# Optimization experiments

Hardware: AMD Instinct MI355X
Metric: run time of the kernel (lower is better)

## Reference

```python
import jax, jax.numpy as jnp
import numpy as np

N, M1, M2 = 8, 512, 512
NITER = 6
LAM = 0.1
BETA = 4096
WL = 6.37e-07  # wavelength constant from expjQz


def _c(x):
    # [..., 2] float (real, imag) -> complex
    return jax.lax.complex(x[..., 0], x[..., 1])


def _ri(x):
    # complex -> [..., 2] float
    return jnp.stack([jnp.real(x), jnp.imag(x)], axis=-1)


def _fft2(x):
    return jnp.fft.fft2(x, axes=(-2, -1))


def _ifft2(x):
    return jnp.fft.ifft2(x, axes=(-2, -1))


def _conv(x, T):
    # Convolve.apply: frequency-domain multiplication by transfer function T (M1,M2)
    return _ifft2(_fft2(x) * T)


def _normalize(x):
    # project onto unit magnitude (phase-only), guarding zero magnitude
    m = jnp.abs(x)
    return x / jnp.where(m == 0, 1.0, m)


def _forward(inp, Q, z):
    # T = exp(1j * z/WL * Q), the expjQz transfer function
    T = jnp.exp(1j * (z / WL) * Q)  # complex64, (M1, M2)
    H = _c(inp)                      # (N, M1, M2) complex measurements
    B = _fft2(jnp.ones((N, M1, M2), jnp.complex64))   # B0 = fft2(ones)
    X = jnp.zeros((N, M1, M2), jnp.complex64)          # X0 = 0
    W = jnp.ones((N, M1, M2), jnp.complex64)           # W0 = 1
    for i in range(NITER):
        convXT = _conv(X, T)
        W = _normalize(convXT + _ifft2(B))
        Qc = H * W
        B = _fft2(Qc - convXT)
        # top-beta magnitude support selection on flattened |B|
        vals, _ = jax.lax.top_k(jnp.abs(B).reshape(-1), BETA)
        thr = vals[-1]
        B = B * (jnp.abs(B) >= thr)
        inp1 = _conv(Qc - _ifft2(B), jnp.conj(T))
        if i < NITER - 1:
            X = inp1 * (jnp.abs(inp1) > LAM)
        else:
            X = inp1
    return W, B


def setup_inputs() -> dict:
    key = jax.random.key(0)
    k1, k2 = jax.random.split(key)
    inp = jax.random.normal(k1, (N, M1, M2, 2), dtype=jnp.float32)
    Q = jax.random.normal(k2, (M1, M2), dtype=jnp.float32)
    z = jnp.float32(1e-06)
    return {"input": inp, "Q": Q, "z": z}


def reference(input, Q, z):
    W, B = _forward(input, Q, z)
    # return real/imag-stacked outputs (aux_W, squeeze(aux_B))
    return _ri(W).astype(jnp.float32), _ri(B).astype(jnp.float32)
```

## Files before the change

### kernel.cpp

```cpp
#include <hip/hip_runtime.h>
#include <math.h>

#define NIMG 8
#define MDIM 512
#define IMGE (MDIM*MDIM)
#define TOT  (NIMG*IMGE)
#define BETA_K 4096
#define LAMD 0.1

typedef double2 c64;

struct SelState { unsigned int known; unsigned int rank; unsigned int thrkey; };

__device__ __forceinline__ int LPOS(int ln, int q){
    return (ln << 9) + (q ^ ((((q >> 4) ^ (2 * ln)) & 7) << 1));
}
__device__ __forceinline__ int rev8(int n){
    return ((n & 7) << 6) | (n & 56) | (n >> 6);
}
__device__ __forceinline__ int rde(int w, int k){
    return 64*k + 8*(w & 7) + (w >> 3);
}

template<bool INV>
__device__ __forceinline__ void dft8(double* xr, double* xi){
    const double C = 0.70710678118654752440;
    double t0r=xr[0]+xr[4], t0i=xi[0]+xi[4];
    double t1r=xr[0]-xr[4], t1i=xi[0]-xi[4];
    double t2r=xr[2]+xr[6], t2i=xi[2]+xi[6];
    double t3r=xr[2]-xr[6], t3i=xi[2]-xi[6];
    double m3r = INV ? -t3i : t3i;
    double m3i = INV ?  t3r : -t3r;
    double E0r=t0r+t2r, E0i=t0i+t2i;
    double E2r=t0r-t2r, E2i=t0i-t2i;
    double E1r=t1r+m3r, E1i=t1i+m3i;
    double E3r=t1r-m3r, E3i=t1i-m3i;
    double u0r=xr[1]+xr[5], u0i=xi[1]+xi[5];
    double u1r=xr[1]-xr[5], u1i=xi[1]-xi[5];
    double u2r=xr[3]+xr[7], u2i=xi[3]+xi[7];
    double u3r=xr[3]-xr[7], u3i=xi[3]-xi[7];
    double n3r = INV ? -u3i : u3i;
    double n3i = INV ?  u3r : -u3r;
    double O0r=u0r+u2r, O0i=u0i+u2i;
    double O2r=u0r-u2r, O2i=u0i-u2i;
    double O1r=u1r+n3r, O1i=u1i+n3i;
    double O3r=u1r-n3r, O3i=u1i-n3i;
    double W1r = INV ? C*(O1r - O1i) : C*(O1r + O1i);
    double W1i = INV ? C*(O1r + O1i) : C*(O1i - O1r);
    double W2r = INV ? -O2i : O2i;
    double W2i = INV ?  O2r : -O2r;
    double W3r = INV ? -C*(O3r + O3i) : C*(O3i - O3r);
    double W3i = INV ?  C*(O3r - O3i) : -C*(O3r + O3i);
    xr[0]=E0r+O0r; xi[0]=E0i+O0i;  xr[4]=E0r-O0r; xi[4]=E0i-O0i;
    xr[1]=E1r+W1r; xi[1]=E1i+W1i;  xr[5]=E1r-W1r; xi[5]=E1i-W1i;
    xr[2]=E2r+W2r; xi[2]=E2i+W2i;  xr[6]=E2r-W2r; xi[6]=E2i-W2i;
    xr[3]=E3r+W3r; xi[3]=E3i+W3i;  xr[7]=E3r-W3r; xi[7]=E3i-W3i;
}

template<bool INV>
__device__ __forceinline__ void dit_from_regs(double (&ar)[2][8], double (&ai)[2][8],
                                              double* re, double* im, const c64* __restrict__ tw){
    const int t=threadIdx.x, w=t&63, l0=t>>6;
    #pragma unroll
    for (int h=0;h<2;++h){
        dft8<INV>(ar[h], ai[h]);
        const int ln=l0+4*h;
        #pragma unroll
        for (int k=0;k<8;++k){ int p=LPOS(ln,8*w+k); re[p]=ar[h][k]; im[p]=ai[h][k]; }
    }
    __syncthreads();
    {
        const int g=w>>3, j=w&7;
        double wr[8], wi[8];
        #pragma unroll
        for (int k=1;k<8;++k){ c64 tv=tw[8*j*k]; wr[k]=tv.x; wi[k]=INV?-tv.y:tv.y; }
        #pragma unroll
        for (int h=0;h<2;++h){
            const int ln=l0+4*h;
            double xr[8], xi[8];
            #pragma unroll
            for (int k=0;k<8;++k){ int p=LPOS(ln,64*g+j+8*k); double a=re[p],b=im[p];
                if(k==0){xr[0]=a; xi[0]=b;} else {xr[k]=a*wr[k]-b*wi[k]; xi[k]=a*wi[k]+b*wr[k];} }
            dft8<INV>(xr,xi);
            #pragma unroll
            for (int k=0;k<8;++k){ int p=LPOS(ln,64*g+j+8*k); re[p]=xr[k]; im[p]=xi[k]; }
        }
    }
    __syncthreads();
    {
        const int j=w;
        double wr[8], wi[8];
        #pragma unroll
        for (int k=1;k<8;++k){ c64 tv=tw[j*k]; wr[k]=tv.x; wi[k]=INV?-tv.y:tv.y; }
        #pragma unroll
        for (int h=0;h<2;++h){
            const int ln=l0+4*h;
            #pragma unroll
            for (int k=0;k<8;++k){ int p=LPOS(ln,j+64*k); double a=re[p],b=im[p];
                if(k==0){ar[h][0]=a; ai[h][0]=b;} else {ar[h][k]=a*wr[k]-b*wi[k]; ai[h][k]=a*wi[k]+b*wr[k];} }
            dft8<INV>(ar[h], ai[h]);
        }
    }
}

template<bool INV>
__device__ __forceinline__ void dif_to_regs(double (&ar)[2][8], double (&ai)[2][8],
                                            double* re, double* im, const c64* __restrict__ tw){
    const int t=threadIdx.x, w=t&63, l0=t>>6;
    {
        const int j=w;
        double wr[8], wi[8];
        #pragma unroll
        for (int k=1;k<8;++k){ c64 tv=tw[j*k]; wr[k]=tv.x; wi[k]=INV?-tv.y:tv.y; }
        #pragma unroll
        for (int h=0;h<2;++h){
            dft8<INV>(ar[h], ai[h]);
            const int ln=l0+4*h;
            #pragma unroll
            for (int k=0;k<8;++k){
                int p=LPOS(ln,j+64*k);
                if(k==0){ re[p]=ar[h][0]; im[p]=ai[h][0]; }
                else { re[p]=ar[h][k]*wr[k]-ai[h][k]*wi[k]; im[p]=ar[h][k]*wi[k]+ai[h][k]*wr[k]; }
            }
        }
    }
    __syncthreads();
    {
        const int g=w>>3, j=w&7;
        double wr[8], wi[8];
        #pragma unroll
        for (int k=1;k<8;++k){ c64 tv=tw[8*j*k]; wr[k]=tv.x; wi[k]=INV?-tv.y:tv.y; }
        #pragma unroll
        for (int h=0;h<2;++h){
            const int ln=l0+4*h;
            double xr[8], xi[8];
            #pragma unroll
            for (int k=0;k<8;++k){ int p=LPOS(ln,64*g+j+8*k); xr[k]=re[p]; xi[k]=im[p]; }
            dft8<INV>(xr,xi);
            #pragma unroll
            for (int k=0;k<8;++k){
                int p=LPOS(ln,64*g+j+8*k);
                if(k==0){ re[p]=xr[0]; im[p]=xi[0]; }
                else { re[p]=xr[k]*wr[k]-xi[k]*wi[k]; im[p]=xr[k]*wi[k]+xi[k]*wr[k]; }
            }
        }
    }
    __syncthreads();
    #pragma unroll
    for (int h=0;h<2;++h){
        const int ln=l0+4*h;
        #pragma unroll
        for (int k=0;k<8;++k){ int p=LPOS(ln,8*w+k); ar[h][k]=re[p]; ai[h][k]=im[p]; }
        dft8<INV>(ar[h], ai[h]);
    }
}

template<bool INV>
__device__ void r8_dit(double* re, double* im, const c64* __restrict__ tw){
    const int t = threadIdx.x;
    const int w = t & 63;
    const int l0 = t >> 6;
    __syncthreads();
    #pragma unroll
    for (int h = 0; h < 2; ++h){
        const int ln = l0 + 4*h;
        double xr[8], xi[8];
        #pragma unroll
        for (int k = 0; k < 8; ++k){ int p = LPOS(ln, 8*w + k); xr[k]=re[p]; xi[k]=im[p]; }
        dft8<INV>(xr, xi);
        #pragma unroll
        for (int k = 0; k < 8; ++k){ int p = LPOS(ln, 8*w + k); re[p]=xr[k]; im[p]=xi[k]; }
    }
    {
        const int g = w >> 3, j = w & 7;
        double wr[8], wi[8];
        #pragma unroll
        for (int k = 1; k < 8; ++k){ c64 tv = tw[8*j*k]; wr[k]=tv.x; wi[k]= INV ? -tv.y : tv.y; }
        __syncthreads();
        #pragma unroll
        for (int h = 0; h < 2; ++h){
            const int ln = l0 + 4*h;
            double xr[8], xi[8];
            #pragma unroll
            for (int k = 0; k < 8; ++k){
                int p = LPOS(ln, 64*g + j + 8*k); double ar=re[p], ai=im[p];
                if (k == 0){ xr[0]=ar; xi[0]=ai; }
                else { xr[k]=ar*wr[k]-ai*wi[k]; xi[k]=ar*wi[k]+ai*wr[k]; }
            }
            dft8<INV>(xr, xi);
            #pragma unroll
            for (int k = 0; k < 8; ++k){ int p = LPOS(ln, 64*g + j + 8*k); re[p]=xr[k]; im[p]=xi[k]; }
        }
    }
    {
        const int j = w;
        double wr[8], wi[8];
        #pragma unroll
        for (int k = 1; k < 8; ++k){ c64 tv = tw[j*k]; wr[k]=tv.x; wi[k]= INV ? -tv.y : tv.y; }
        __syncthreads();
        #pragma unroll
        for (int h = 0; h < 2; ++h){
            const int ln = l0 + 4*h;
            double xr[8], xi[8];
            #pragma unroll
            for (int k = 0; k < 8; ++k){
                int p = LPOS(ln, j + 64*k); double ar=re[p], ai=im[p];
                if (k == 0){ xr[0]=ar; xi[0]=ai; }
                else { xr[k]=ar*wr[k]-ai*wi[k]; xi[k]=ar*wi[k]+ai*wr[k]; }
            }
            dft8<INV>(xr, xi);
            #pragma unroll
            for (int k = 0; k < 8; ++k){ int p = LPOS(ln, j + 64*k); re[p]=xr[k]; im[p]=xi[k]; }
        }
    }
}

template<bool INV>
__device__ void r8_dif(double* re, double* im, const c64* __restrict__ tw){
    const int t = threadIdx.x;
    const int w = t & 63;
    const int l0 = t >> 6;
    {
        const int j = w;
        double wr[8], wi[8];
        #pragma unroll
        for (int k = 1; k < 8; ++k){ c64 tv = tw[j*k]; wr[k]=tv.x; wi[k]= INV ? -tv.y : tv.y; }
        __syncthreads();
        #pragma unroll
        for (int h = 0; h < 2; ++h){
            const int ln = l0 + 4*h;
            double xr[8], xi[8];
            #pragma unroll
            for (int k = 0; k < 8; ++k){ int p = LPOS(ln, j + 64*k); xr[k]=re[p]; xi[k]=im[p]; }
            dft8<INV>(xr, xi);
            #pragma unroll
            for (int k = 0; k < 8; ++k){
                int p = LPOS(ln, j + 64*k);
                if (k == 0){ re[p]=xr[0]; im[p]=xi[0]; }
                else { re[p]=xr[k]*wr[k]-xi[k]*wi[k]; im[p]=xr[k]*wi[k]+xi[k]*wr[k]; }
            }
        }
    }
    {
        const int g = w >> 3, j = w & 7;
        double wr[8], wi[8];
        #pragma unroll
        for (int k = 1; k < 8; ++k){ c64 tv = tw[8*j*k]; wr[k]=tv.x; wi[k]= INV ? -tv.y : tv.y; }
        __syncthreads();
        #pragma unroll
        for (int h = 0; h < 2; ++h){
            const int ln = l0 + 4*h;
            double xr[8], xi[8];
            #pragma unroll
            for (int k = 0; k < 8; ++k){ int p = LPOS(ln, 64*g + j + 8*k); xr[k]=re[p]; xi[k]=im[p]; }
            dft8<INV>(xr, xi);
            #pragma unroll
            for (int k = 0; k < 8; ++k){
                int p = LPOS(ln, 64*g + j + 8*k);
                if (k == 0){ re[p]=xr[0]; im[p]=xi[0]; }
                else { re[p]=xr[k]*wr[k]-xi[k]*wi[k]; im[p]=xr[k]*wi[k]+xi[k]*wr[k]; }
            }
        }
    }
    __syncthreads();
    #pragma unroll
    for (int h = 0; h < 2; ++h){
        const int ln = l0 + 4*h;
        double xr[8], xi[8];
        #pragma unroll
        for (int k = 0; k < 8; ++k){ int p = LPOS(ln, 8*w + k); xr[k]=re[p]; xi[k]=im[p]; }
        dft8<INV>(xr, xi);
        #pragma unroll
        for (int k = 0; k < 8; ++k){ int p = LPOS(ln, 8*w + k); re[p]=xr[k]; im[p]=xi[k]; }
    }
}

__device__ __forceinline__ void col_load32(const float2* __restrict__ src, size_t base,
                                           double* re, double* im){
    const int t = threadIdx.x;
    #pragma unroll
    for (int it = 0; it < 16; ++it){
        int idx = it*256 + t; int ln = idx & 7, e = idx >> 3;
        float2 v = src[base + ln + (size_t)e*512];
        int p = LPOS(ln, rev8(e));
        re[p] = (double)v.x; im[p] = (double)v.y;
    }
}

__global__ __launch_bounds__(256) void k_init(const float* __restrict__ Q,
                                              const float* __restrict__ zp,
                                              c64* __restrict__ T,
                                              c64* __restrict__ tw){
    int i = blockIdx.x*256 + threadIdx.x;
    if (i < IMGE){
        double a = ((double)zp[0] / 6.37e-07) * (double)Q[i];
        T[i] = make_double2(cos(a), sin(a));
    }
    if (i < 512){
        double a = -6.283185307179586476925286766559 * ((double)i / 512.0);
        tw[i] = make_double2(cos(a), sin(a));
    }
}

__global__ __launch_bounds__(256,2) void k_colF(const float2* __restrict__ H,
                                                float2* __restrict__ t2,
                                                const c64* __restrict__ tw){
    __shared__ double re[4096]; __shared__ double im[4096];
    const int t = threadIdx.x, blk = blockIdx.x;
    const size_t base = (size_t)(blk >> 6) * IMGE + (size_t)(blk & 63) * 8;
    col_load32(H, base, re, im);
    r8_dit<false>(re, im, tw);
    __syncthreads();
    #pragma unroll
    for (int it = 0; it < 16; ++it){
        int idx = it*256 + t; int ln = idx & 7, e = idx >> 3;
        int p = LPOS(ln, e);
        t2[base + ln + (size_t)e*512] = make_float2((float)re[p], (float)im[p]);
    }
}

__global__ __launch_bounds__(256,2) void k_rowA(const float2* __restrict__ B,
                                                const unsigned int* __restrict__ keys,
                                                const SelState* __restrict__ st,
                                                const float2* __restrict__ G,
                                                float2* __restrict__ t2,
                                                const c64* __restrict__ tw){
    __shared__ double re[4096]; __shared__ double im[4096];
    const int t = threadIdx.x, blk = blockIdx.x;
    const int w = t & 63, l0 = t >> 6;
    const size_t base = (size_t)blk * 4096;
    const unsigned int thr = st->thrkey;
    double ar[2][8], ai[2][8];
    #pragma unroll
    for (int h=0;h<2;++h){ const int ln=l0+4*h;
        #pragma unroll
        for (int k=0;k<8;++k){
            size_t addr = base + ln*512 + (w + 64*k);
            float2 g = G[addr];
            float2 b = B[addr];
            bool keep = keys[addr] >= thr;
            ar[h][k] = (double)g.x + (keep ? (double)b.x : 0.0);
            ai[h][k] = (double)g.y + (keep ? (double)b.y : 0.0);
        } }
    dif_to_regs<true>(ar, ai, re, im, tw);
    const double sc = 1.0/512.0;
    #pragma unroll
    for (int h=0;h<2;++h){ const int ln=l0+4*h;
        #pragma unroll
        for (int k=0;k<8;++k)
            t2[base + ln*512 + rde(w,k)] = make_float2((float)(ar[h][k]*sc), (float)(ai[h][k]*sc)); }
}

template<bool FINAL>
__global__ __launch_bounds__(256,2) void k_colWQ(float2* __restrict__ t2,
                                                 const float2* __restrict__ H,
                                                 float2* __restrict__ outW,
                                                 const c64* __restrict__ tw){
    __shared__ double re[4096]; __shared__ double im[4096];
    const int t = threadIdx.x, blk = blockIdx.x;
    const size_t base = (size_t)(blk >> 6) * IMGE + (size_t)(blk & 63) * 8;
    col_load32(t2, base, re, im);
    r8_dit<true>(re, im, tw);
    __syncthreads();
    const double sc = 1.0/512.0;
    #pragma unroll
    for (int it = 0; it < 16; ++it){
        int idx = it*256 + t; int ln = idx & 7, e = idx >> 3;
        size_t addr = base + ln + (size_t)e*512;
        int p = LPOS(ln, e);
        double zr = re[p]*sc, zi = im[p]*sc;
        double m = sqrt(zr*zr + zi*zi);
        double d = (m == 0.0) ? 1.0 : m;
        double wx = zr/d, wy = zi/d;
        if (FINAL) outW[addr] = make_float2((float)wx, (float)wy);
        float2 h = H[addr];
        re[p] = (double)h.x*wx - (double)h.y*wy;
        im[p] = (double)h.x*wy + (double)h.y*wx;
    }
    r8_dif<false>(re, im, tw);
    __syncthreads();
    #pragma unroll
    for (int it = 0; it < 16; ++it){
        int idx = it*256 + t; int ln = idx & 7, e = idx >> 3;
        int p = LPOS(ln, rev8(e));
        t2[base + ln + (size_t)e*512] = make_float2((float)re[p], (float)im[p]);
    }
}

template<bool G0>
__global__ __launch_bounds__(256,2) void k_rowC(const float2* __restrict__ t2,
                                                const float2* __restrict__ G,
                                                float2* __restrict__ B,
                                                unsigned int* __restrict__ keys,
                                                unsigned int* __restrict__ hist,
                                                const c64* __restrict__ tw){
    __shared__ double re[4096]; __shared__ double im[4096];
    const int t = threadIdx.x, blk = blockIdx.x;
    const int w = t & 63, l0 = t >> 6;
    const size_t base = (size_t)blk * 4096;
    double ar[2][8], ai[2][8];
    #pragma unroll
    for (int h=0;h<2;++h){ const int ln=l0+4*h;
        #pragma unroll
        for (int k=0;k<8;++k){ float2 v = t2[base + ln*512 + rde(w,k)];
            ar[h][k]=(double)v.x; ai[h][k]=(double)v.y; } }
    dit_from_regs<false>(ar, ai, re, im, tw);
    __syncthreads();
    unsigned int* lh = reinterpret_cast<unsigned int*>(re);
    for (int b = t; b < 2048; b += 256) lh[b] = 0u;
    __syncthreads();
    #pragma unroll
    for (int h=0;h<2;++h){
        const int ln=l0+4*h;
        #pragma unroll
        for (int k=0;k<8;++k){
            size_t addr = base + ln*512 + (w + 64*k);
            double br = ar[h][k], bi = ai[h][k];
            if (!G0){ float2 g = G[addr]; br -= (double)g.x; bi -= (double)g.y; }
            B[addr] = make_float2((float)br, (float)bi);
            unsigned int key = __float_as_uint((float)sqrt(br*br + bi*bi));
            keys[addr] = key;
            atomicAdd(&lh[key >> 21], 1u);
        }
    }
    __syncthreads();
    for (int b = t; b < 2048; b += 256){
        unsigned int v = lh[b];
        if (v) atomicAdd(&hist[b], v);
    }
}

template<bool G0>
__global__ __launch_bounds__(256,2) void k_rowD(const float2* __restrict__ B,
                                                const unsigned int* __restrict__ keys,
                                                const SelState* __restrict__ st,
                                                const float2* __restrict__ G,
                                                const c64* __restrict__ T,
                                                float2* __restrict__ t2,
                                                const c64* __restrict__ tw){
    __shared__ double re[4096]; __shared__ double im[4096];
    const int t = threadIdx.x, blk = blockIdx.x;
    const int w = t & 63, l0 = t >> 6;
    const size_t base = (size_t)blk * 4096;
    const unsigned int thr = st->thrkey;
    double ar[2][8], ai[2][8];
    #pragma unroll
    for (int h=0;h<2;++h){
        const int ln=l0+4*h;
        const int u = (blk & 63) * 8 + ln;
        #pragma unroll
        for (int k=0;k<8;++k){
            const int e = w + 64*k;
            size_t addr = base + ln*512 + e;
            float2 b = B[addr];
            bool lo = keys[addr] < thr;
            double vr = lo ? (double)b.x : 0.0;
            double vi = lo ? (double)b.y : 0.0;
            if (!G0){ float2 g = G[addr]; vr += (double)g.x; vi += (double)g.y; }
            c64 tv = T[u*512 + e];
            ar[h][k] = vr*tv.x + vi*tv.y;
            ai[h][k] = vi*tv.x - vr*tv.y;
        }
    }
    dif_to_regs<true>(ar, ai, re, im, tw);
    const double sc = 1.0/512.0;
    #pragma unroll
    for (int h=0;h<2;++h){ const int ln=l0+4*h;
        #pragma unroll
        for (int k=0;k<8;++k)
            t2[base + ln*512 + rde(w,k)] = make_float2((float)(ar[h][k]*sc), (float)(ai[h][k]*sc)); }
}

__global__ __launch_bounds__(256,2) void k_colX(float2* __restrict__ t2,
                                                const c64* __restrict__ tw){
    __shared__ double re[4096]; __shared__ double im[4096];
    const int t = threadIdx.x, blk = blockIdx.x;
    const size_t base = (size_t)(blk >> 6) * IMGE + (size_t)(blk & 63) * 8;
    col_load32(t2, base, re, im);
    r8_dit<true>(re, im, tw);
    __syncthreads();
    const double sc = 1.0/512.0;
    #pragma unroll
    for (int it = 0; it < 16; ++it){
        int idx = it*256 + t;
        int p = LPOS(idx & 7, idx >> 3);
        double vr = re[p]*sc, vi = im[p]*sc;
        double m = sqrt(vr*vr + vi*vi);
        bool keep = m > LAMD;
        re[p] = keep ? vr : 0.0;
        im[p] = keep ? vi : 0.0;
    }
    r8_dif<false>(re, im, tw);
    __syncthreads();
    #pragma unroll
    for (int it = 0; it < 16; ++it){
        int idx = it*256 + t; int ln = idx & 7, e = idx >> 3;
        int p = LPOS(ln, rev8(e));
        t2[base + ln + (size_t)e*512] = make_float2((float)re[p], (float)im[p]);
    }
}

__global__ __launch_bounds__(256,2) void k_rowF(const float2* __restrict__ t2,
                                                const c64* __restrict__ T,
                                                float2* __restrict__ G,
                                                const c64* __restrict__ tw){
    __shared__ double re[4096]; __shared__ double im[4096];
    const int t = threadIdx.x, blk = blockIdx.x;
    const int w = t & 63, l0 = t >> 6;
    const size_t base = (size_t)blk * 4096;
    double ar[2][8], ai[2][8];
    #pragma unroll
    for (int h=0;h<2;++h){ const int ln=l0+4*h;
        #pragma unroll
        for (int k=0;k<8;++k){ float2 v = t2[base + ln*512 + rde(w,k)];
            ar[h][k]=(double)v.x; ai[h][k]=(double)v.y; } }
    dit_from_regs<false>(ar, ai, re, im, tw);
    #pragma unroll
    for (int h=0;h<2;++h){
        const int ln=l0+4*h;
        const int u = (blk & 63) * 8 + ln;
        #pragma unroll
        for (int k=0;k<8;++k){
            const int e = w + 64*k;
            size_t addr = base + ln*512 + e;
            c64 tv = T[u*512 + e];
            double xr = ar[h][k], xi = ai[h][k];
            G[addr] = make_float2((float)(xr*tv.x - xi*tv.y), (float)(xr*tv.y + xi*tv.x));
        }
    }
}

__global__ __launch_bounds__(256) void k_outB(const float2* __restrict__ B,
                                              const unsigned int* __restrict__ keys,
                                              const SelState* __restrict__ st,
                                              float2* __restrict__ outB){
    int i = blockIdx.x*256 + threadIdx.x;
    float2 v = B[i];
    if (keys[i] < st->thrkey) v = make_float2(0.0f, 0.0f);
    outB[i] = v;
}

__global__ __launch_bounds__(256) void k_hist(const unsigned int* __restrict__ keys,
                                              unsigned int* __restrict__ hist,
                                              const SelState* __restrict__ st,
                                              int shiftHi, int shift, int dbits){
    __shared__ unsigned int lh[2048];
    int t = threadIdx.x;
    int nd = 1 << dbits;
    for (int b = t; b < nd; b += 256) lh[b] = 0u;
    __syncthreads();
    unsigned known = st->known;
    unsigned msk = (unsigned)((1u << dbits) - 1u);
    for (int i = blockIdx.x*256 + t; i < TOT; i += gridDim.x*256){
        unsigned k = keys[i];
        if ((k >> shiftHi) == known) atomicAdd(&lh[(k >> shift) & msk], 1u);
    }
    __syncthreads();
    for (int b = t; b < nd; b += 256){
        unsigned v = lh[b];
        if (v) atomicAdd(&hist[b], v);
    }
}

__global__ __launch_bounds__(256) void k_scan(unsigned int* __restrict__ hist,
                                              SelState* __restrict__ st,
                                              int dbits, int mode){
    __shared__ unsigned int s[256];
    const int t = threadIdx.x;
    const int nd = 1 << dbits;
    const int per = nd >> 8;
    unsigned c[8];
    unsigned local = 0u;
    const int b0 = t * per;
    #pragma unroll
    for (int j = 0; j < 8; ++j){
        unsigned v = 0u;
        if (j < per){ v = hist[b0 + j]; hist[b0 + j] = 0u; }
        c[j] = v; local += v;
    }
    unsigned rank = (mode == 2) ? (unsigned)BETA_K : st->rank;
    s[t] = local;
    __syncthreads();
    #pragma unroll
    for (int off = 1; off < 256; off <<= 1){
        unsigned add = (t + off < 256) ? s[t + off] : 0u;
        __syncthreads();
        s[t] += add;
        __syncthreads();
    }
    unsigned stot   = s[t];
    unsigned sAfter = (t < 255) ? s[t + 1] : 0u;
    if (sAfter < rank && stot >= rank){
        unsigned cum = sAfter;
        int j = per - 1;
        #pragma unroll
        for (int k = 7; k >= 0; --k){
            if (k > per - 1) continue;
            j = k;
            if (cum + c[k] >= rank) break;
            cum += c[k];
        }
        st->rank = rank - cum;
        unsigned kn = (mode == 2) ? 0u : st->known;
        unsigned nk = (kn << dbits) | (unsigned)(b0 + j);
        st->known = nk;
        if (mode == 1) st->thrkey = nk;
    }
}

extern "C" void kernel_launch(void* const* d_in, const int* in_sizes, int n_in,
                              void* d_out, int out_size, void* d_ws, size_t ws_size,
                              hipStream_t stream){
    (void)in_sizes; (void)n_in; (void)out_size; (void)ws_size;
    const float2* H = (const float2*)d_in[0];
    const float*  Q = (const float*)d_in[1];
    const float*  zp = (const float*)d_in[2];

    char* ws = (char*)d_ws;
    const size_t A = (size_t)TOT * sizeof(float2);
    float2* t2 = (float2*)(ws);
    float2* B  = (float2*)(ws + A);
    float2* G  = (float2*)(ws + 2*A);
    unsigned int* keys = (unsigned int*)(ws + 3*A);
    c64* T  = (c64*)(ws + 3*A + (size_t)TOT*4);
    c64* tw = (c64*)(ws + 3*A + (size_t)TOT*4 + (size_t)IMGE*16);
    unsigned int* hist = (unsigned int*)((char*)tw + 512*16);
    SelState* st = (SelState*)((char*)hist + 8192);

    float2* outW = (float2*)d_out;
    float2* outB = ((float2*)d_out) + TOT;

    hipMemsetAsync(hist, 0, 2048*sizeof(unsigned int), stream);
    k_init<<<IMGE/256, 256, 0, stream>>>(Q, zp, T, tw);

    auto sel = [&](){
        k_scan<<<1,256,0,stream>>>(hist, st, 11, 2);
        k_hist<<<1024,256,0,stream>>>(keys, hist, st, 21, 10, 11);
        k_scan<<<1,256,0,stream>>>(hist, st, 11, 0);
        k_hist<<<1024,256,0,stream>>>(keys, hist, st, 10, 0, 10);
        k_scan<<<1,256,0,stream>>>(hist, st, 10, 1);
    };

    k_colF<<<512,256,0,stream>>>(H, t2, tw);
    k_rowC<true><<<512,256,0,stream>>>(t2, G, B, keys, hist, tw);
    sel();
    k_rowD<true><<<512,256,0,stream>>>(B, keys, st, G, T, t2, tw);
    k_colX<<<512,256,0,stream>>>(t2, tw);
    k_rowF<<<512,256,0,stream>>>(t2, T, G, tw);

    for (int iter = 2; iter <= 5; ++iter){
        k_rowA<<<512,256,0,stream>>>(B, keys, st, G, t2, tw);
        k_colWQ<false><<<512,256,0,stream>>>(t2, H, outW, tw);
        k_rowC<false><<<512,256,0,stream>>>(t2, G, B, keys, hist, tw);
        sel();
        k_rowD<false><<<512,256,0,stream>>>(B, keys, st, G, T, t2, tw);
        k_colX<<<512,256,0,stream>>>(t2, tw);
        k_rowF<<<512,256,0,stream>>>(t2, T, G, tw);
    }

    k_rowA<<<512,256,0,stream>>>(B, keys, st, G, t2, tw);
    k_colWQ<true><<<512,256,0,stream>>>(t2, H, outW, tw);
    k_rowC<false><<<512,256,0,stream>>>(t2, G, B, keys, hist, tw);
    sel();
    k_outB<<<TOT/256,256,0,stream>>>(B, keys, st, outB);
}
```

Measured before the change: 770.1 us.

## Fuse rowF into rowA, merge histogram+scan via last-block, use 512-thread FFT blocks

Merges the rowF and rowA kernels into one k_rowFA, so the G round trip and one launch per iteration go away. The separate histogram and scan kernels are combined into k_hist_scan, where the last block to finish does the scan, found with an atomic counter. The first select pass appears to be folded into rowC. FFT kernels now launch 512 threads with one line per thread instead of 256 threads with two lines each, which raises parallelism but may increase register pressure per wave. The goal is fewer launches and fewer global passes, in exchange for relying on threadfence and atomic last-block logic.

```diff
diff --git a/kernel.cpp b/kernel.cpp
--- a/kernel.cpp
+++ b/kernel.cpp
@@ -58,33 +58,25 @@
 }
 
 template<bool INV>
-__device__ __forceinline__ void dit_from_regs(double (&ar)[2][8], double (&ai)[2][8],
+__device__ __forceinline__ void dit_from_regs(double (&ar)[8], double (&ai)[8],
                                               double* re, double* im, const c64* __restrict__ tw){
-    const int t=threadIdx.x, w=t&63, l0=t>>6;
-    #pragma unroll
-    for (int h=0;h<2;++h){
-        dft8<INV>(ar[h], ai[h]);
-        const int ln=l0+4*h;
-        #pragma unroll
-        for (int k=0;k<8;++k){ int p=LPOS(ln,8*w+k); re[p]=ar[h][k]; im[p]=ai[h][k]; }
-    }
+    const int t=threadIdx.x, w=t&63, ln=t>>6;
+    dft8<INV>(ar, ai);
+    #pragma unroll
+    for (int k=0;k<8;++k){ int p=LPOS(ln,8*w+k); re[p]=ar[k]; im[p]=ai[k]; }
     __syncthreads();
     {
         const int g=w>>3, j=w&7;
         double wr[8], wi[8];
         #pragma unroll
         for (int k=1;k<8;++k){ c64 tv=tw[8*j*k]; wr[k]=tv.x; wi[k]=INV?-tv.y:tv.y; }
-        #pragma unroll
-        for (int h=0;h<2;++h){
-            const int ln=l0+4*h;
-            double xr[8], xi[8];
-            #pragma unroll
-            for (int k=0;k<8;++k){ int p=LPOS(ln,64*g+j+8*k); double a=re[p],b=im[p];
-                if(k==0){xr[0]=a; xi[0]=b;} else {xr[k]=a*wr[k]-b*wi[k]; xi[k]=a*wi[k]+b*wr[k];} }
-            dft8<INV>(xr,xi);
-            #pragma unroll
-            for (int k=0;k<8;++k){ int p=LPOS(ln,64*g+j+8*k); re[p]=xr[k]; im[p]=xi[k]; }
-        }
+        double xr[8], xi[8];
+        #pragma unroll
+        for (int k=0;k<8;++k){ int p=LPOS(ln,64*g+j+8*k); double a=re[p],b=im[p];
+            if(k==0){xr[0]=a; xi[0]=b;} else {xr[k]=a*wr[k]-b*wi[k]; xi[k]=a*wi[k]+b*wr[k];} }
+        dft8<INV>(xr,xi);
+        #pragma unroll
+        for (int k=0;k<8;++k){ int p=LPOS(ln,64*g+j+8*k); re[p]=xr[k]; im[p]=xi[k]; }
     }
     __syncthreads();
     {
@@ -93,35 +85,27 @@
         #pragma unroll
         for (int k=1;k<8;++k){ c64 tv=tw[j*k]; wr[k]=tv.x; wi[k]=INV?-tv.y:tv.y; }
         #pragma unroll
-        for (int h=0;h<2;++h){
-            const int ln=l0+4*h;
-            #pragma unroll
-            for (int k=0;k<8;++k){ int p=LPOS(ln,j+64*k); double a=re[p],b=im[p];
-                if(k==0){ar[h][0]=a; ai[h][0]=b;} else {ar[h][k]=a*wr[k]-b*wi[k]; ai[h][k]=a*wi[k]+b*wr[k];} }
-            dft8<INV>(ar[h], ai[h]);
-        }
+        for (int k=0;k<8;++k){ int p=LPOS(ln,j+64*k); double a=re[p],b=im[p];
+            if(k==0){ar[0]=a; ai[0]=b;} else {ar[k]=a*wr[k]-b*wi[k]; ai[k]=a*wi[k]+b*wr[k];} }
+        dft8<INV>(ar, ai);
     }
 }
 
 template<bool INV>
-__device__ __forceinline__ void dif_to_regs(double (&ar)[2][8], double (&ai)[2][8],
+__device__ __forceinline__ void dif_to_regs(double (&ar)[8], double (&ai)[8],
                                             double* re, double* im, const c64* __restrict__ tw){
-    const int t=threadIdx.x, w=t&63, l0=t>>6;
+    const int t=threadIdx.x, w=t&63, ln=t>>6;
     {
         const int j=w;
         double wr[8], wi[8];
         #pragma unroll
         for (int k=1;k<8;++k){ c64 tv=tw[j*k]; wr[k]=tv.x; wi[k]=INV?-tv.y:tv.y; }
-        #pragma unroll
-        for (int h=0;h<2;++h){
-            dft8<INV>(ar[h], ai[h]);
-            const int ln=l0+4*h;
-            #pragma unroll
-            for (int k=0;k<8;++k){
-                int p=LPOS(ln,j+64*k);
-                if(k==0){ re[p]=ar[h][0]; im[p]=ai[h][0]; }
-                else { re[p]=ar[h][k]*wr[k]-ai[h][k]*wi[k]; im[p]=ar[h][k]*wi[k]+ai[h][k]*wr[k]; }
-            }
+        dft8<INV>(ar, ai);
+        #pragma unroll
+        for (int k=0;k<8;++k){
+            int p=LPOS(ln,j+64*k);
+            if(k==0){ re[p]=ar[0]; im[p]=ai[0]; }
+            else { re[p]=ar[k]*wr[k]-ai[k]*wi[k]; im[p]=ar[k]*wi[k]+ai[k]*wr[k]; }
         }
     }
     __syncthreads();
@@ -130,40 +114,28 @@
         double wr[8], wi[8];
         #pragma unroll
         for (int k=1;k<8;++k){ c64 tv=tw[8*j*k]; wr[k]=tv.x; wi[k]=INV?-tv.y:tv.y; }
-        #pragma unroll
-        for (int h=0;h<2;++h){
-            const int ln=l0+4*h;
-            double xr[8], xi[8];
-            #pragma unroll
-            for (int k=0;k<8;++k){ int p=LPOS(ln,64*g+j+8*k); xr[k]=re[p]; xi[k]=im[p]; }
-            dft8<INV>(xr,xi);
-            #pragma unroll
-            for (int k=0;k<8;++k){
-                int p=LPOS(ln,64*g+j+8*k);
-                if(k==0){ re[p]=xr[0]; im[p]=xi[0]; }
-                else { re[p]=xr[k]*wr[k]-xi[k]*wi[k]; im[p]=xr[k]*wi[k]+xi[k]*wr[k]; }
-            }
-        }
-    }
-    __syncthreads();
-    #pragma unroll
-    for (int h=0;h<2;++h){
-        const int ln=l0+4*h;
-        #pragma unroll
-        for (int k=0;k<8;++k){ int p=LPOS(ln,8*w+k); ar[h][k]=re[p]; ai[h][k]=im[p]; }
-        dft8<INV>(ar[h], ai[h]);
-    }
+        double xr[8], xi[8];
+        #pragma unroll
+        for (int k=0;k<8;++k){ int p=LPOS(ln,64*g+j+8*k); xr[k]=re[p]; xi[k]=im[p]; }
+        dft8<INV>(xr,xi);
+        #pragma unroll
+        for (int k=0;k<8;++k){
+            int p=LPOS(ln,64*g+j+8*k);
+            if(k==0){ re[p]=xr[0]; im[p]=xi[0]; }
+            else { re[p]=xr[k]*wr[k]-xi[k]*wi[k]; im[p]=xr[k]*wi[k]+xi[k]*wr[k]; }
+        }
+    }
+    __syncthreads();
+    #pragma unroll
+    for (int k=0;k<8;++k){ int p=LPOS(ln,8*w+k); ar[k]=re[p]; ai[k]=im[p]; }
+    dft8<INV>(ar, ai);
 }
 
 template<bool INV>
 __device__ void r8_dit(double* re, double* im, const c64* __restrict__ tw){
-    const int t = threadIdx.x;
-    const int w = t & 63;
-    const int l0 = t >> 6;
-    __syncthreads();
-    #pragma unroll
-    for (int h = 0; h < 2; ++h){
-        const int ln = l0 + 4*h;
+    const int t = threadIdx.x, w = t & 63, ln = t >> 6;
+    __syncthreads();
+    {
         double xr[8], xi[8];
         #pragma unroll
         for (int k = 0; k < 8; ++k){ int p = LPOS(ln, 8*w + k); xr[k]=re[p]; xi[k]=im[p]; }
@@ -177,20 +149,16 @@
         #pragma unroll
         for (int k = 1; k < 8; ++k){ c64 tv = tw[8*j*k]; wr[k]=tv.x; wi[k]= INV ? -tv.y : tv.y; }
         __syncthreads();
-        #pragma unroll
-        for (int h = 0; h < 2; ++h){
-            const int ln = l0 + 4*h;
-            double xr[8], xi[8];
-            #pragma unroll
-            for (int k = 0; k < 8; ++k){
-                int p = LPOS(ln, 64*g + j + 8*k); double ar=re[p], ai=im[p];
-                if (k == 0){ xr[0]=ar; xi[0]=ai; }
-                else { xr[k]=ar*wr[k]-ai*wi[k]; xi[k]=ar*wi[k]+ai*wr[k]; }
-            }
-            dft8<INV>(xr, xi);
-            #pragma unroll
-            for (int k = 0; k < 8; ++k){ int p = LPOS(ln, 64*g + j + 8*k); re[p]=xr[k]; im[p]=xi[k]; }
-        }
+        double xr[8], xi[8];
+        #pragma unroll
+        for (int k = 0; k < 8; ++k){
+            int p = LPOS(ln, 64*g + j + 8*k); double a=re[p], b=im[p];
+            if (k == 0){ xr[0]=a; xi[0]=b; }
+            else { xr[k]=a*wr[k]-b*wi[k]; xi[k]=a*wi[k]+b*wr[k]; }
+        }
+        dft8<INV>(xr, xi);
+        #pragma unroll
+        for (int k = 0; k < 8; ++k){ int p = LPOS(ln, 64*g + j + 8*k); re[p]=xr[k]; im[p]=xi[k]; }
     }
     {
         const int j = w;
@@ -198,47 +166,37 @@
         #pragma unroll
         for (int k = 1; k < 8; ++k){ c64 tv = tw[j*k]; wr[k]=tv.x; wi[k]= INV ? -tv.y : tv.y; }
         __syncthreads();
-        #pragma unroll
-        for (int h = 0; h < 2; ++h){
-            const int ln = l0 + 4*h;
-            double xr[8], xi[8];
-            #pragma unroll
-            for (int k = 0; k < 8; ++k){
-                int p = LPOS(ln, j + 64*k); double ar=re[p], ai=im[p];
-                if (k == 0){ xr[0]=ar; xi[0]=ai; }
-                else { xr[k]=ar*wr[k]-ai*wi[k]; xi[k]=ar*wi[k]+ai*wr[k]; }
-            }
-            dft8<INV>(xr, xi);
-            #pragma unroll
-            for (int k = 0; k < 8; ++k){ int p = LPOS(ln, j + 64*k); re[p]=xr[k]; im[p]=xi[k]; }
-        }
+        double xr[8], xi[8];
+        #pragma unroll
+        for (int k = 0; k < 8; ++k){
+            int p = LPOS(ln, j + 64*k); double a=re[p], b=im[p];
+            if (k == 0){ xr[0]=a; xi[0]=b; }
+            else { xr[k]=a*wr[k]-b*wi[k]; xi[k]=a*wi[k]+b*wr[k]; }
+        }
+        dft8<INV>(xr, xi);
+        #pragma unroll
+        for (int k = 0; k < 8; ++k){ int p = LPOS(ln, j + 64*k); re[p]=xr[k]; im[p]=xi[k]; }
     }
 }
 
 template<bool INV>
 __device__ void r8_dif(double* re, double* im, const c64* __restrict__ tw){
-    const int t = threadIdx.x;
-    const int w = t & 63;
-    const int l0 = t >> 6;
+    const int t = threadIdx.x, w = t & 63, ln = t >> 6;
     {
         const int j = w;
         double wr[8], wi[8];
         #pragma unroll
         for (int k = 1; k < 8; ++k){ c64 tv = tw[j*k]; wr[k]=tv.x; wi[k]= INV ? -tv.y : tv.y; }
         __syncthreads();
-        #pragma unroll
-        for (int h = 0; h < 2; ++h){
-            const int ln = l0 + 4*h;
-            double xr[8], xi[8];
-            #pragma unroll
-            for (int k = 0; k < 8; ++k){ int p = LPOS(ln, j + 64*k); xr[k]=re[p]; xi[k]=im[p]; }
-            dft8<INV>(xr, xi);
-            #pragma unroll
-            for (int k = 0; k < 8; ++k){
-                int p = LPOS(ln, j + 64*k);
-                if (k == 0){ re[p]=xr[0]; im[p]=xi[0]; }
-                else { re[p]=xr[k]*wr[k]-xi[k]*wi[k]; im[p]=xr[k]*wi[k]+xi[k]*wr[k]; }
-            }
+        double xr[8], xi[8];
+        #pragma unroll
+        for (int k = 0; k < 8; ++k){ int p = LPOS(ln, j + 64*k); xr[k]=re[p]; xi[k]=im[p]; }
+        dft8<INV>(xr, xi);
+        #pragma unroll
+        for (int k = 0; k < 8; ++k){
+            int p = LPOS(ln, j + 64*k);
+            if (k == 0){ re[p]=xr[0]; im[p]=xi[0]; }
+            else { re[p]=xr[k]*wr[k]-xi[k]*wi[k]; im[p]=xr[k]*wi[k]+xi[k]*wr[k]; }
         }
     }
     {
@@ -247,25 +205,19 @@
         #pragma unroll
         for (int k = 1; k < 8; ++k){ c64 tv = tw[8*j*k]; wr[k]=tv.x; wi[k]= INV ? -tv.y : tv.y; }
         __syncthreads();
-        #pragma unroll
-        for (int h = 0; h < 2; ++h){
-            const int ln = l0 + 4*h;
-            double xr[8], xi[8];
-            #pragma unroll
-            for (int k = 0; k < 8; ++k){ int p = LPOS(ln, 64*g + j + 8*k); xr[k]=re[p]; xi[k]=im[p]; }
-            dft8<INV>(xr, xi);
-            #pragma unroll
-            for (int k = 0; k < 8; ++k){
-                int p = LPOS(ln, 64*g + j + 8*k);
-                if (k == 0){ re[p]=xr[0]; im[p]=xi[0]; }
-                else { re[p]=xr[k]*wr[k]-xi[k]*wi[k]; im[p]=xr[k]*wi[k]+xi[k]*wr[k]; }
-            }
-        }
-    }
-    __syncthreads();
-    #pragma unroll
-    for (int h = 0; h < 2; ++h){
-        const int ln = l0 + 4*h;
+        double xr[8], xi[8];
+        #pragma unroll
+        for (int k = 0; k < 8; ++k){ int p = LPOS(ln, 64*g + j + 8*k); xr[k]=re[p]; xi[k]=im[p]; }
+        dft8<INV>(xr, xi);
+        #pragma unroll
+        for (int k = 0; k < 8; ++k){
+            int p = LPOS(ln, 64*g + j + 8*k);
+            if (k == 0){ re[p]=xr[0]; im[p]=xi[0]; }
+            else { re[p]=xr[k]*wr[k]-xi[k]*wi[k]; im[p]=xr[k]*wi[k]+xi[k]*wr[k]; }
+        }
+    }
+    __syncthreads();
+    {
         double xr[8], xi[8];
         #pragma unroll
         for (int k = 0; k < 8; ++k){ int p = LPOS(ln, 8*w + k); xr[k]=re[p]; xi[k]=im[p]; }
@@ -279,12 +231,71 @@
                                            double* re, double* im){
     const int t = threadIdx.x;
     #pragma unroll
-    for (int it = 0; it < 16; ++it){
-        int idx = it*256 + t; int ln = idx & 7, e = idx >> 3;
+    for (int it = 0; it < 8; ++it){
+        int idx = it*512 + t; int ln = idx & 7, e = idx >> 3;
         float2 v = src[base + ln + (size_t)e*512];
         int p = LPOS(ln, rev8(e));
         re[p] = (double)v.x; im[p] = (double)v.y;
     }
+}
+
+__device__ __forceinline__ void scan_block(unsigned* __restrict__ hist,
+                                           SelState* __restrict__ st,
+                                           unsigned* sBuf, int dbits, int mode){
+    const int t = threadIdx.x;
+    const int per = (1 << dbits) >> 8;
+    unsigned c[8]; unsigned local = 0u; const int b0 = t * per;
+    if (t < 256){
+        #pragma unroll
+        for (int j = 0; j < 8; ++j){
+            unsigned v = 0u;
+            if (j < per) v = atomicExch(&hist[b0 + j], 0u);
+            c[j] = v; local += v;
+        }
+        sBuf[t] = local;
+    }
+    unsigned rank = (mode == 2) ? (unsigned)BETA_K : st->rank;
+    __syncthreads();
+    for (int off = 1; off < 256; off <<= 1){
+        unsigned add = 0u;
+        if (t < 256 && t + off < 256) add = sBuf[t + off];
+        __syncthreads();
+        if (t < 256) sBuf[t] += add;
+        __syncthreads();
+    }
+    if (t < 256){
+        unsigned stot   = sBuf[t];
+        unsigned sAfter = (t < 255) ? sBuf[t + 1] : 0u;
+        if (sAfter < rank && stot >= rank){
+            unsigned cum = sAfter;
+            int j = per - 1;
+            #pragma unroll
+            for (int k = 7; k >= 0; --k){
+                if (k > per - 1) continue;
+                j = k;
+                if (cum + c[k] >= rank) break;
+                cum += c[k];
+            }
+            st->rank = rank - cum;
+            unsigned kn = (mode == 2) ? 0u : st->known;
+            unsigned nk = (kn << dbits) | (unsigned)(b0 + j);
+            st->known = nk;
+            if (mode == 1) st->thrkey = nk;
+        }
+    }
+}
+
+__device__ __forceinline__ bool is_last_block(unsigned* __restrict__ cnt,
+                                              unsigned* flagLds, int target){
+    __threadfence();
+    if (threadIdx.x == 0){
+        unsigned old = atomicAdd(cnt, 1u);
+        unsigned f = (old == (unsigned)(target - 1)) ? 1u : 0u;
+        if (f) atomicExch(cnt, 0u);
+        *flagLds = f;
+    }
+    __syncthreads();
+    return *flagLds != 0u;
 }
 
 __global__ __launch_bounds__(256) void k_init(const float* __restrict__ Q,
@@ -302,7 +313,7 @@
     }
 }
 
-__global__ __launch_bounds__(256,2) void k_colF(const float2* __restrict__ H,
+__global__ __launch_bounds__(512,4) void k_colF(const float2* __restrict__ H,
                                                 float2* __restrict__ t2,
                                                 const c64* __restrict__ tw){
     __shared__ double re[4096]; __shared__ double im[4096];
@@ -312,47 +323,54 @@
     r8_dit<false>(re, im, tw);
     __syncthreads();
     #pragma unroll
-    for (int it = 0; it < 16; ++it){
-        int idx = it*256 + t; int ln = idx & 7, e = idx >> 3;
+    for (int it = 0; it < 8; ++it){
+        int idx = it*512 + t; int ln = idx & 7, e = idx >> 3;
         int p = LPOS(ln, e);
         t2[base + ln + (size_t)e*512] = make_float2((float)re[p], (float)im[p]);
     }
 }
 
-__global__ __launch_bounds__(256,2) void k_rowA(const float2* __restrict__ B,
-                                                const unsigned int* __restrict__ keys,
-                                                const SelState* __restrict__ st,
-                                                const float2* __restrict__ G,
-                                                float2* __restrict__ t2,
-                                                const c64* __restrict__ tw){
+__global__ __launch_bounds__(512,4) void k_rowFA(float2* __restrict__ t2,
+                                                 const float2* __restrict__ B,
+                                                 const unsigned int* __restrict__ keys,
+                                                 const SelState* __restrict__ st,
+                                                 const c64* __restrict__ T,
+                                                 float2* __restrict__ G,
+                                                 const c64* __restrict__ tw){
     __shared__ double re[4096]; __shared__ double im[4096];
     const int t = threadIdx.x, blk = blockIdx.x;
-    const int w = t & 63, l0 = t >> 6;
+    const int w = t & 63, ln = t >> 6;
     const size_t base = (size_t)blk * 4096;
     const unsigned int thr = st->thrkey;
-    double ar[2][8], ai[2][8];
-    #pragma unroll
-    for (int h=0;h<2;++h){ const int ln=l0+4*h;
-        #pragma unroll
-        for (int k=0;k<8;++k){
-            size_t addr = base + ln*512 + (w + 64*k);
-            float2 g = G[addr];
-            float2 b = B[addr];
-            bool keep = keys[addr] >= thr;
-            ar[h][k] = (double)g.x + (keep ? (double)b.x : 0.0);
-            ai[h][k] = (double)g.y + (keep ? (double)b.y : 0.0);
-        } }
+    double ar[8], ai[8];
+    #pragma unroll
+    for (int k=0;k<8;++k){ float2 v = t2[base + ln*512 + rde(w,k)];
+        ar[k]=(double)v.x; ai[k]=(double)v.y; }
+    dit_from_regs<false>(ar, ai, re, im, tw);
+    const int u = (blk & 63) * 8 + ln;
+    #pragma unroll
+    for (int k=0;k<8;++k){
+        const int e = w + 64*k;
+        size_t addr = base + ln*512 + e;
+        c64 tv = T[u*512 + e];
+        double xr = ar[k], xi = ai[k];
+        double gr = xr*tv.x - xi*tv.y;
+        double gi = xr*tv.y + xi*tv.x;
+        G[addr] = make_float2((float)gr, (float)gi);
+        float2 b = B[addr];
+        bool keep = keys[addr] >= thr;
+        ar[k] = gr + (keep ? (double)b.x : 0.0);
+        ai[k] = gi + (keep ? (double)b.y : 0.0);
+    }
     dif_to_regs<true>(ar, ai, re, im, tw);
     const double sc = 1.0/512.0;
     #pragma unroll
-    for (int h=0;h<2;++h){ const int ln=l0+4*h;
-        #pragma unroll
-        for (int k=0;k<8;++k)
-            t2[base + ln*512 + rde(w,k)] = make_float2((float)(ar[h][k]*sc), (float)(ai[h][k]*sc)); }
+    for (int k=0;k<8;++k)
+        t2[base + ln*512 + rde(w,k)] = make_float2((float)(ar[k]*sc), (float)(ai[k]*sc));
 }
 
 template<bool FINAL>
-__global__ __launch_bounds__(256,2) void k_colWQ(float2* __restrict__ t2,
+__global__ __launch_bounds__(512,4) void k_colWQ(float2* __restrict__ t2,
                                                  const float2* __restrict__ H,
                                                  float2* __restrict__ outW,
                                                  const c64* __restrict__ tw){
@@ -364,8 +382,8 @@
     __syncthreads();
     const double sc = 1.0/512.0;
     #pragma unroll
-    for (int it = 0; it < 16; ++it){
-        int idx = it*256 + t; int ln = idx & 7, e = idx >> 3;
+    for (int it = 0; it < 8; ++it){
+        int idx = it*512 + t; int ln = idx & 7, e = idx >> 3;
         size_t addr = base + ln + (size_t)e*512;
         int p = LPOS(ln, e);
         double zr = re[p]*sc, zi = im[p]*sc;
@@ -380,58 +398,59 @@
     r8_dif<false>(re, im, tw);
     __syncthreads();
     #pragma unroll
-    for (int it = 0; it < 16; ++it){
-        int idx = it*256 + t; int ln = idx & 7, e = idx >> 3;
+    for (int it = 0; it < 8; ++it){
+        int idx = it*512 + t; int ln = idx & 7, e = idx >> 3;
         int p = LPOS(ln, rev8(e));
         t2[base + ln + (size_t)e*512] = make_float2((float)re[p], (float)im[p]);
     }
 }
 
 template<bool G0>
-__global__ __launch_bounds__(256,2) void k_rowC(const float2* __restrict__ t2,
+__global__ __launch_bounds__(512,4) void k_rowC(const float2* __restrict__ t2,
                                                 const float2* __restrict__ G,
                                                 float2* __restrict__ B,
                                                 unsigned int* __restrict__ keys,
                                                 unsigned int* __restrict__ hist,
+                                                unsigned int* __restrict__ cnt,
+                                                SelState* __restrict__ st,
                                                 const c64* __restrict__ tw){
     __shared__ double re[4096]; __shared__ double im[4096];
     const int t = threadIdx.x, blk = blockIdx.x;
-    const int w = t & 63, l0 = t >> 6;
+    const int w = t & 63, ln = t >> 6;
     const size_t base = (size_t)blk * 4096;
-    double ar[2][8], ai[2][8];
-    #pragma unroll
-    for (int h=0;h<2;++h){ const int ln=l0+4*h;
-        #pragma unroll
-        for (int k=0;k<8;++k){ float2 v = t2[base + ln*512 + rde(w,k)];
-            ar[h][k]=(double)v.x; ai[h][k]=(double)v.y; } }
+    double ar[8], ai[8];
+    #pragma unroll
+    for (int k=0;k<8;++k){ float2 v = t2[base + ln*512 + rde(w,k)];
+        ar[k]=(double)v.x; ai[k]=(double)v.y; }
     dit_from_regs<false>(ar, ai, re, im, tw);
     __syncthreads();
     unsigned int* lh = reinterpret_cast<unsigned int*>(re);
-    for (int b = t; b < 2048; b += 256) lh[b] = 0u;
-    __syncthreads();
-    #pragma unroll
-    for (int h=0;h<2;++h){
-        const int ln=l0+4*h;
-        #pragma unroll
-        for (int k=0;k<8;++k){
-            size_t addr = base + ln*512 + (w + 64*k);
-            double br = ar[h][k], bi = ai[h][k];
-            if (!G0){ float2 g = G[addr]; br -= (double)g.x; bi -= (double)g.y; }
-            B[addr] = make_float2((float)br, (float)bi);
-            unsigned int key = __float_as_uint((float)sqrt(br*br + bi*bi));
-            keys[addr] = key;
-            atomicAdd(&lh[key >> 21], 1u);
-        }
-    }
-    __syncthreads();
-    for (int b = t; b < 2048; b += 256){
+    unsigned int* sBuf = reinterpret_cast<unsigned int*>(im);
+    unsigned int* flag = sBuf + 256;
+    for (int b = t; b < 2048; b += 512) lh[b] = 0u;
+    __syncthreads();
+    #pragma unroll
+    for (int k=0;k<8;++k){
+        size_t addr = base + ln*512 + (w + 64*k);
+        double br = ar[k], bi = ai[k];
+        if (!G0){ float2 g = G[addr]; br -= (double)g.x; bi -= (double)g.y; }
+        B[addr] = make_float2((float)br, (float)bi);
+        unsigned int key = __float_as_uint((float)sqrt(br*br + bi*bi));
+        keys[addr] = key;
+        atomicAdd(&lh[key >> 21], 1u);
+    }
+    __syncthreads();
+    for (int b = t; b < 2048; b += 512){
         unsigned int v = lh[b];
         if (v) atomicAdd(&hist[b], v);
     }
+    if (is_last_block(cnt, flag, gridDim.x)){
+        scan_block(hist, st, sBuf, 11, 2);
+    }
 }
 
 template<bool G0>
-__global__ __launch_bounds__(256,2) void k_rowD(const float2* __restrict__ B,
+__global__ __launch_bounds__(512,4) void k_rowD(const float2* __restrict__ B,
                                                 const unsigned int* __restrict__ keys,
                                                 const SelState* __restrict__ st,
                                                 const float2* __restrict__ G,
@@ -440,38 +459,32 @@
                                                 const c64* __restrict__ tw){
     __shared__ double re[4096]; __shared__ double im[4096];
     const int t = threadIdx.x, blk = blockIdx.x;
-    const int w = t & 63, l0 = t >> 6;
+    const int w = t & 63, ln = t >> 6;
     const size_t base = (size_t)blk * 4096;
     const unsigned int thr = st->thrkey;
-    double ar[2][8], ai[2][8];
-    #pragma unroll
-    for (int h=0;h<2;++h){
-        const int ln=l0+4*h;
-        const int u = (blk & 63) * 8 + ln;
-        #pragma unroll
-        for (int k=0;k<8;++k){
-            const int e = w + 64*k;
-            size_t addr = base + ln*512 + e;
-            float2 b = B[addr];
-            bool lo = keys[addr] < thr;
-            double vr = lo ? (double)b.x : 0.0;
-            double vi = lo ? (double)b.y : 0.0;
-            if (!G0){ float2 g = G[addr]; vr += (double)g.x; vi += (double)g.y; }
-            c64 tv = T[u*512 + e];
-            ar[h][k] = vr*tv.x + vi*tv.y;
-            ai[h][k] = vi*tv.x - vr*tv.y;
-        }
+    const int u = (blk & 63) * 8 + ln;
+    double ar[8], ai[8];
+    #pragma unroll
+    for (int k=0;k<8;++k){
+        const int e = w + 64*k;
+        size_t addr = base + ln*512 + e;
+        float2 b = B[addr];
+        bool lo = keys[addr] < thr;
+        double vr = lo ? (double)b.x : 0.0;
+        double vi = lo ? (double)b.y : 0.0;
+        if (!G0){ float2 g = G[addr]; vr += (double)g.x; vi += (double)g.y; }
+        c64 tv = T[u*512 + e];
+        ar[k] = vr*tv.x + vi*tv.y;
+        ai[k] = vi*tv.x - vr*tv.y;
     }
     dif_to_regs<true>(ar, ai, re, im, tw);
     const double sc = 1.0/512.0;
     #pragma unroll
-    for (int h=0;h<2;++h){ const int ln=l0+4*h;
-        #pragma unroll
-        for (int k=0;k<8;++k)
-            t2[base + ln*512 + rde(w,k)] = make_float2((float)(ar[h][k]*sc), (float)(ai[h][k]*sc)); }
-}
-
-__global__ __launch_bounds__(256,2) void k_colX(float2* __restrict__ t2,
+    for (int k=0;k<8;++k)
+        t2[base + ln*512 + rde(w,k)] = make_float2((float)(ar[k]*sc), (float)(ai[k]*sc));
+}
+
+__global__ __launch_bounds__(512,4) void k_colX(float2* __restrict__ t2,
                                                 const c64* __restrict__ tw){
     __shared__ double re[4096]; __shared__ double im[4096];
     const int t = threadIdx.x, blk = blockIdx.x;
@@ -481,8 +494,8 @@
     __syncthreads();
     const double sc = 1.0/512.0;
     #pragma unroll
-    for (int it = 0; it < 16; ++it){
-        int idx = it*256 + t;
+    for (int it = 0; it < 8; ++it){
+        int idx = it*512 + t;
         int p = LPOS(idx & 7, idx >> 3);
         double vr = re[p]*sc, vi = im[p]*sc;
         double m = sqrt(vr*vr + vi*vi);
@@ -493,40 +506,38 @@
     r8_dif<false>(re, im, tw);
     __syncthreads();
     #pragma unroll
-    for (int it = 0; it < 16; ++it){
-        int idx = it*256 + t; int ln = idx & 7, e = idx >> 3;
+    for (int it = 0; it < 8; ++it){
+        int idx = it*512 + t; int ln = idx & 7, e = idx >> 3;
         int p = LPOS(ln, rev8(e));
         t2[base + ln + (size_t)e*512] = make_float2((float)re[p], (float)im[p]);
     }
 }
 
-__global__ __launch_bounds__(256,2) void k_rowF(const float2* __restrict__ t2,
-                                                const c64* __restrict__ T,
-                                                float2* __restrict__ G,
-                                                const c64* __restrict__ tw){
-    __shared__ double re[4096]; __shared__ double im[4096];
-    const int t = threadIdx.x, blk = blockIdx.x;
-    const int w = t & 63, l0 = t >> 6;
-    const size_t base = (size_t)blk * 4096;
-    double ar[2][8], ai[2][8];
-    #pragma unroll
-    for (int h=0;h<2;++h){ const int ln=l0+4*h;
-        #pragma unroll
-        for (int k=0;k<8;++k){ float2 v = t2[base + ln*512 + rde(w,k)];
-            ar[h][k]=(double)v.x; ai[h][k]=(double)v.y; } }
-    dit_from_regs<false>(ar, ai, re, im, tw);
-    #pragma unroll
-    for (int h=0;h<2;++h){
-        const int ln=l0+4*h;
-        const int u = (blk & 63) * 8 + ln;
-        #pragma unroll
-        for (int k=0;k<8;++k){
-            const int e = w + 64*k;
-            size_t addr = base + ln*512 + e;
-            c64 tv = T[u*512 + e];
-            double xr = ar[h][k], xi = ai[h][k];
-            G[addr] = make_float2((float)(xr*tv.x - xi*tv.y), (float)(xr*tv.y + xi*tv.x));
-        }
+__global__ __launch_bounds__(256) void k_hist_scan(const unsigned int* __restrict__ keys,
+                                                   unsigned int* __restrict__ hist,
+                                                   unsigned int* __restrict__ cnt,
+                                                   SelState* __restrict__ st,
+                                                   int shiftHi, int shift, int dbits, int mode){
+    __shared__ unsigned int lh[2048];
+    __shared__ unsigned int sBuf[256];
+    __shared__ unsigned int flag;
+    int t = threadIdx.x;
+    int nd = 1 << dbits;
+    for (int b = t; b < nd; b += 256) lh[b] = 0u;
+    __syncthreads();
+    unsigned known = st->known;
+    unsigned msk = (unsigned)((1u << dbits) - 1u);
+    for (int i = blockIdx.x*256 + t; i < TOT; i += gridDim.x*256){
+        unsigned k = keys[i];
+        if ((k >> shiftHi) == known) atomicAdd(&lh[(k >> shift) & msk], 1u);
+    }
+    __syncthreads();
+    for (int b = t; b < nd; b += 256){
+        unsigned v = lh[b];
+        if (v) atomicAdd(&hist[b], v);
+    }
+    if (is_last_block(cnt, &flag, gridDim.x)){
+        scan_block(hist, st, sBuf, dbits, mode);
     }
 }
 
@@ -538,74 +549,6 @@
     float2 v = B[i];
     if (keys[i] < st->thrkey) v = make_float2(0.0f, 0.0f);
     outB[i] = v;
-}
-
-__global__ __launch_bounds__(256) void k_hist(const unsigned int* __restrict__ keys,
-                                              unsigned int* __restrict__ hist,
-                                              const SelState* __restrict__ st,
-                                              int shiftHi, int shift, int dbits){
-    __shared__ unsigned int lh[2048];
-    int t = threadIdx.x;
-    int nd = 1 << dbits;
-    for (int b = t; b < nd; b += 256) lh[b] = 0u;
-    __syncthreads();
-    unsigned known = st->known;
-    unsigned msk = (unsigned)((1u << dbits) - 1u);
-    for (int i = blockIdx.x*256 + t; i < TOT; i += gridDim.x*256){
-        unsigned k = keys[i];
-        if ((k >> shiftHi) == known) atomicAdd(&lh[(k >> shift) & msk], 1u);
-    }
-    __syncthreads();
-    for (int b = t; b < nd; b += 256){
-        unsigned v = lh[b];
-        if (v) atomicAdd(&hist[b], v);
-    }
-}
-
-__global__ __launch_bounds__(256) void k_scan(unsigned int* __restrict__ hist,
-                                              SelState* __restrict__ st,
-                                              int dbits, int mode){
-    __shared__ unsigned int s[256];
-    const int t = threadIdx.x;
-    const int nd = 1 << dbits;
-    const int per = nd >> 8;
-    unsigned c[8];
-    unsigned local = 0u;
-    const int b0 = t * per;
-    #pragma unroll
-    for (int j = 0; j < 8; ++j){
-        unsigned v = 0u;
-        if (j < per){ v = hist[b0 + j]; hist[b0 + j] = 0u; }
-        c[j] = v; local += v;
-    }
-    unsigned rank = (mode == 2) ? (unsigned)BETA_K : st->rank;
-    s[t] = local;
-    __syncthreads();
-    #pragma unroll
-    for (int off = 1; off < 256; off <<= 1){
-        unsigned add = (t + off < 256) ? s[t + off] : 0u;
-        __syncthreads();
-        s[t] += add;
-        __syncthreads();
-    }
-    unsigned stot   = s[t];
-    unsigned sAfter = (t < 255) ? s[t + 1] : 0u;
-    if (sAfter < rank && stot >= rank){
-        unsigned cum = sAfter;
-        int j = per - 1;
-        #pragma unroll
-        for (int k = 7; k >= 0; --k){
-            if (k > per - 1) continue;
-            j = k;
-            if (cum + c[k] >= rank) break;
-            cum += c[k];
-        }
-        st->rank = rank - cum;
-        unsigned kn = (mode == 2) ? 0u : st->known;
-        unsigned nk = (kn << dbits) | (unsigned)(b0 + j);
-        st->known = nk;
-        if (mode == 1) st->thrkey = nk;
-    }
 }
 
 extern "C" void kernel_launch(void* const* d_in, const int* in_sizes, int n_in,
@@ -625,42 +568,38 @@
     c64* T  = (c64*)(ws + 3*A + (size_t)TOT*4);
     c64* tw = (c64*)(ws + 3*A + (size_t)TOT*4 + (size_t)IMGE*16);
     unsigned int* hist = (unsigned int*)((char*)tw + 512*16);
-    SelState* st = (SelState*)((char*)hist + 8192);
+    unsigned int* cnt  = (unsigned int*)((char*)hist + 8192);
+    SelState* st = (SelState*)((char*)hist + 8192 + 64);
 
     float2* outW = (float2*)d_out;
     float2* outB = ((float2*)d_out) + TOT;
 
-    hipMemsetAsync(hist, 0, 2048*sizeof(unsigned int), stream);
+    hipMemsetAsync(hist, 0, 8192 + 64, stream);
     k_init<<<IMGE/256, 256, 0, stream>>>(Q, zp, T, tw);
 
-    auto sel = [&](){
-        k_scan<<<1,256,0,stream>>>(hist, st, 11, 2);
-        k_hist<<<1024,256,0,stream>>>(keys, hist, st, 21, 10, 11);
-        k_scan<<<1,256,0,stream>>>(hist, st, 11, 0);
-        k_hist<<<1024,256,0,stream>>>(keys, hist, st, 10, 0, 10);
-        k_scan<<<1,256,0,stream>>>(hist, st, 10, 1);
+    auto sel23 = [&](){
+        k_hist_scan<<<512,256,0,stream>>>(keys, hist, cnt, st, 21, 10, 11, 0);
+        k_hist_scan<<<512,256,0,stream>>>(keys, hist, cnt, st, 10,  0, 10, 1);
     };
 
-    k_colF<<<512,256,0,stream>>>(H, t2, tw);
-    k_rowC<true><<<512,256,0,stream>>>(t2, G, B, keys, hist, tw);
-    sel();
-    k_rowD<true><<<512,256,0,stream>>>(B, keys, st, G, T, t2, tw);
-    k_colX<<<512,256,0,stream>>>(t2, tw);
-    k_rowF<<<512,256,0,stream>>>(t2, T, G, tw);
+    k_colF<<<512,512,0,stream>>>(H, t2, tw);
+    k_rowC<true><<<512,512,0,stream>>>(t2, G, B, keys, hist, cnt, st, tw);
+    sel23();
+    k_rowD<true><<<512,512,0,stream>>>(B, keys, st, G, T, t2, tw);
+    k_colX<<<512,512,0,stream>>>(t2, tw);
 
     for (int iter = 2; iter <= 5; ++iter){
-        k_rowA<<<512,256,0,stream>>>(B, keys, st, G, t2, tw);
-        k_colWQ<false><<<512,256,0,stream>>>(t2, H, outW, tw);
-        k_rowC<false><<<512,256,0,stream>>>(t2, G, B, keys, hist, tw);
-        sel();
-        k_rowD<false><<<512,256,0,stream>>>(B, keys, st, G, T, t2, tw);
-        k_colX<<<512,256,0,stream>>>(t2, tw);
-        k_rowF<<<512,256,0,stream>>>(t2, T, G, tw);
-    }
-
-    k_rowA<<<512,256,0,stream>>>(B, keys, st, G, t2, tw);
-    k_colWQ<true><<<512,256,0,stream>>>(t2, H, outW, tw);
-    k_rowC<false><<<512,256,0,stream>>>(t2, G, B, keys, hist, tw);
-    sel();
+        k_rowFA<<<512,512,0,stream>>>(t2, B, keys, st, T, G, tw);
+        k_colWQ<false><<<512,512,0,stream>>>(t2, H, outW, tw);
+        k_rowC<false><<<512,512,0,stream>>>(t2, G, B, keys, hist, cnt, st, tw);
+        sel23();
+        k_rowD<false><<<512,512,0,stream>>>(B, keys, st, G, T, t2, tw);
+        k_colX<<<512,512,0,stream>>>(t2, tw);
+    }
+
+    k_rowFA<<<512,512,0,stream>>>(t2, B, keys, st, T, G, tw);
+    k_colWQ<true><<<512,512,0,stream>>>(t2, H, outW, tw);
+    k_rowC<false><<<512,512,0,stream>>>(t2, G, B, keys, hist, cnt, st, tw);
+    sel23();
     k_outB<<<TOT/256,256,0,stream>>>(B, keys, st, outB);
 }
```

After: 1.732 ms. +124.9%, slower.
